# Performance work log

Hardware: AMD Instinct MI355X
Metric: run time of the kernel (lower is better)

The kernel has to match this reference:

```python
import jax, jax.numpy as jnp
import numpy as np

BETA = 0.25  # commitment weight per level (vqconfig default)
EPS = 1e-12  # F.normalize eps


def setup_inputs() -> dict:
    key = jax.random.key(0)
    k1, k2 = jax.random.split(key)
    z = jax.random.normal(k1, (4, 256, 32, 32), dtype=jnp.float32)
    cb = jax.random.normal(k2, (4, 4096, 256), dtype=jnp.float32)
    # embeddings are row-normalized at init in the torch module
    cb = cb / jnp.maximum(jnp.linalg.norm(cb, axis=-1, keepdims=True), EPS)
    return {"z": z, "codebooks": cb}


def _nearest_code(r_flat, embed):
    """use_znorm=True path: cosine-similarity nearest neighbor.
    r_flat: (N, C), embed: (K, C) -> idx: (N,) int32"""
    rn = r_flat / jnp.maximum(jnp.linalg.norm(r_flat, axis=1, keepdims=True), EPS)
    en = embed / jnp.maximum(jnp.linalg.norm(embed, axis=1, keepdims=True), EPS)
    sim = jnp.einsum('nc,kc->nk', rn, en)  # (N, K)
    return jnp.argmax(sim, axis=1)


def reference(z, codebooks):
    """Residual VQ over L codebooks (eval mode: no EMA / kmeans init).
    z: (B, C, H, W); codebooks: (L, K, C).
    Returns (z_q_st (B,C,H,W), indices (L,B,H,W), qloss scalar)."""
    B, C, H, W = z.shape
    L = codebooks.shape[0]
    z_flat = z.transpose(0, 2, 3, 1).reshape(-1, C)  # (N, C)
    residual = z_flat
    q_sum = jnp.zeros_like(z_flat)
    qloss = jnp.zeros((), dtype=z.dtype)
    indices = []
    for l in range(L):  # small fixed level loop with sequential data dependency
        E = codebooks[l]
        idx = _nearest_code(residual, E)          # (N,)
        z_q = E[idx]                              # gather (N, C)
        q_sum = q_sum + z_q
        qloss = qloss + BETA * jnp.mean((jax.lax.stop_gradient(z_q) - residual) ** 2)
        residual = residual - jax.lax.stop_gradient(z_q)
        indices.append(idx.reshape(B, H, W))
    q = q_sum.reshape(B, H, W, C).transpose(0, 3, 1, 2)
    z_q_st = z + jax.lax.stop_gradient(q - z)     # straight-through estimator
    return z_q_st, jnp.stack(indices, axis=0), qloss
```

## Files before the change

kernel.cpp:

```cpp
#include <hip/hip_runtime.h>


#define OFF_AS   0
#define OFF_BS   524288
#define OFF_R    2621440
#define OFF_INV  3670016
#define OFF_PV   3686400
#define OFF_RN   3817472
#define OFF_CNT  3821568
#define OFF_CAND 3825664
#define OFF_CVAL 4874240
#define OFF_SSQ  5922816

#define BETA 0.25f
#define EPSN 1e-12f
#define CAP 256
#define SLC 16
#define OVF (1 << 20)
#define MARGIN 0.012f
#define NEGINF -3.0e38f

typedef __attribute__((ext_vector_type(8))) short short8;
typedef __attribute__((ext_vector_type(4))) float f32x4;

__device__ __forceinline__ unsigned short f2bf(float x) {
  unsigned u = __float_as_uint(x);
  unsigned r = (u + 0x7fffu + ((u >> 16) & 1u)) >> 16;
  return (unsigned short)r;
}

__device__ __forceinline__ void gload16(const void* g, void* s) {
  __builtin_amdgcn_global_load_lds(
      (const __attribute__((address_space(1))) unsigned int*)g,
      (__attribute__((address_space(3))) unsigned int*)s, 16, 0, 0);
}

__global__ __launch_bounds__(256) void k_prep_r(const float* __restrict__ z,
                                                float* __restrict__ r) {
  __shared__ float t[32][33];
  int id = blockIdx.x;
  int b = id >> 8; int rem = id & 255; int ct = rem >> 5; int ht = rem & 31;
  int c0 = ct * 32, h0 = ht * 32;
  int col = threadIdx.x & 31, row0 = threadIdx.x >> 5;
#pragma unroll
  for (int p = 0; p < 4; ++p) {
    int row = row0 + p * 8;
    t[row][col] = z[((b * 256 + c0 + row) << 10) + h0 + col];
  }
  __syncthreads();
#pragma unroll
  for (int p = 0; p < 4; ++p) {
    int row = row0 + p * 8;
    r[(b * 1024 + h0 + row) * 256 + c0 + col] = t[col][row];
  }
}

__global__ __launch_bounds__(256) void k_prep_inv(const float* __restrict__ cb,
                                                  float* __restrict__ inv) {
  int w = threadIdx.x >> 6, lane = threadIdx.x & 63;
  int row = blockIdx.x * 4 + w;
  float4 v = *(const float4*)(cb + row * 256 + lane * 4);
  float s = v.x * v.x + v.y * v.y + v.z * v.z + v.w * v.w;
#pragma unroll
  for (int off = 32; off; off >>= 1) s += __shfl_xor(s, off);
  if (lane == 0) inv[row] = 1.0f / fmaxf(sqrtf(s), EPSN);
}

__global__ __launch_bounds__(256) void k_bsplit_all(const float* __restrict__ cb,
                                                    const float* __restrict__ inv,
                                                    unsigned short* __restrict__ BS) {
  int row = blockIdx.x, c = threadIdx.x;
  float x = cb[(row << 8) + c] * inv[row];
  BS[(row << 8) + c] = f2bf(x);
}

__global__ __launch_bounds__(256) void k_split_a(const float* __restrict__ r,
                                                 unsigned short* __restrict__ AS,
                                                 float* __restrict__ rnorm,
                                                 int* __restrict__ cnt) {
  __shared__ float wsum[4];
  int n = blockIdx.x, tid = threadIdx.x;
  float x = r[(n << 8) + tid];
  AS[(n << 8) + tid] = f2bf(x);
  float sq = x * x;
  int lane = tid & 63, w = tid >> 6;
#pragma unroll
  for (int off = 32; off; off >>= 1) sq += __shfl_xor(sq, off);
  if (lane == 0) wsum[w] = sq;
  __syncthreads();
  if (tid == 0) {
    rnorm[n] = sqrtf((wsum[0] + wsum[1]) + (wsum[2] + wsum[3]));
    cnt[n] = 0;
  }
}

__global__ __launch_bounds__(256) void k_gemm_argmax(
    const unsigned short* __restrict__ AS, const unsigned short* __restrict__ BS,
    float* __restrict__ pval, const float* __restrict__ rnorm,
    int* __restrict__ cnt, int* __restrict__ cand, float* __restrict__ cval) {
  __shared__ unsigned short lA[128 * 64];
  __shared__ unsigned short lB[128 * 64];
  __shared__ float sv[2][2][64];
  __shared__ float scomb[2][64];
  __shared__ float rn_s[2][64];
  __shared__ int   lcnt[128];
  __shared__ int   lck[128][SLC];
  __shared__ float lcv[128][SLC];

  int bid = blockIdx.x;
  int wg = (bid & 7) * 128 + (bid >> 3);
  int bm = wg >> 5, bn = wg & 31;
  int mbase = bm * 128, nbase = bn * 128;
  int tid = threadIdx.x;
  int wid = tid >> 6, ln = tid & 63;
  int wr = wid >> 1, wc = wid & 1;
  int grp = ln >> 4, li = ln & 15;

  f32x4 acc[4][4];
#pragma unroll
  for (int i = 0; i < 4; ++i)
#pragma unroll
    for (int j = 0; j < 4; ++j) acc[i][j] = (f32x4){0.f, 0.f, 0.f, 0.f};

  for (int ks = 0; ks < 4; ++ks) {
    __syncthreads();
    int k0 = ks * 64;
#pragma unroll
    for (int i = 0; i < 4; ++i) {
      int idx = i * 256 + tid;
      int row = idx >> 3, cc = idx & 7;
      int src = cc ^ (row & 7);
      gload16(AS + ((mbase + row) << 8) + k0 + src * 8, ((char*)lA) + idx * 16);
    }
#pragma unroll
    for (int i = 0; i < 4; ++i) {
      int idx = i * 256 + tid;
      int row = idx >> 3, cc = idx & 7;
      int src = cc ^ (row & 7);
      gload16(BS + ((nbase + row) << 8) + k0 + src * 8, ((char*)lB) + idx * 16);
    }
    __syncthreads();
#pragma unroll
    for (int kk = 0; kk < 2; ++kk) {
      short8 b[4];
#pragma unroll
      for (int ni = 0; ni < 4; ++ni) {
        int row = wc * 64 + ni * 16 + li;
        int cc = kk * 4 + grp;
        b[ni] = *(const short8*)(((const char*)lB) + row * 128 + (cc ^ (row & 7)) * 16);
      }
#pragma unroll
      for (int mi = 0; mi < 4; ++mi) {
        int row = wr * 64 + mi * 16 + li;
        int cc = kk * 4 + grp;
        short8 a = *(const short8*)(((const char*)lA) + row * 128 + (cc ^ (row & 7)) * 16);
#pragma unroll
        for (int ni = 0; ni < 4; ++ni)
          acc[mi][ni] = __builtin_amdgcn_mfma_f32_16x16x32_bf16(a, b[ni], acc[mi][ni], 0, 0, 0);
      }
    }
  }

#pragma unroll
  for (int mi = 0; mi < 4; ++mi) {
#pragma unroll
    for (int reg = 0; reg < 4; ++reg) {
      float v = acc[mi][0][reg];
#pragma unroll
      for (int ni = 1; ni < 4; ++ni) v = fmaxf(v, acc[mi][ni][reg]);
#pragma unroll
      for (int off = 1; off < 16; off <<= 1) v = fmaxf(v, __shfl_xor(v, off));
      if (li == 0) sv[wr][wc][mi * 16 + grp * 4 + reg] = v;
    }
  }
  __syncthreads();
  if (tid < 128) {
    int wr2 = tid >> 6, r64 = tid & 63;
    float m = fmaxf(sv[wr2][0][r64], sv[wr2][1][r64]);
    int n = mbase + wr2 * 64 + r64;
    pval[n * 32 + bn] = m;
    scomb[wr2][r64] = m;
    rn_s[wr2][r64] = rnorm[n];
    lcnt[tid] = 0;
  }
  __syncthreads();
#pragma unroll
  for (int mi = 0; mi < 4; ++mi) {
#pragma unroll
    for (int reg = 0; reg < 4; ++reg) {
      int rl = mi * 16 + grp * 4 + reg;
      float thr = scomb[wr][rl] - MARGIN * rn_s[wr][rl];
      int rloc = wr * 64 + rl;
#pragma unroll
      for (int ni = 0; ni < 4; ++ni) {
        float v = acc[mi][ni][reg];
        if (v >= thr) {
          int pos = atomicAdd(&lcnt[rloc], 1);
          if (pos < SLC) {
            lck[rloc][pos] = nbase + wc * 64 + ni * 16 + li;
            lcv[rloc][pos] = v;
          }
        }
      }
    }
  }
  __syncthreads();
  if (tid < 128) {
    int rloc = tid;
    int n = mbase + rloc;
    int raw = lcnt[rloc];
    int lc = raw < SLC ? raw : SLC;
    int add = raw > SLC ? (lc + OVF) : lc;
    if (add > 0) {
      int base = atomicAdd(&cnt[n], add);
      for (int j = 0; j < lc; ++j) {
        int pos = base + j;
        if (pos < CAP) {
          cand[n * CAP + pos] = lck[rloc][j];
          cval[n * CAP + pos] = lcv[rloc][j];
        }
      }
    }
  }
}

__global__ __launch_bounds__(256) void k_refine_update(
    const float* __restrict__ cb, const float* __restrict__ inv,
    float* __restrict__ r, const float* __restrict__ pval,
    float* __restrict__ rnorm, int* __restrict__ cnt,
    const int* __restrict__ cand, const float* __restrict__ cval,
    unsigned short* __restrict__ AS, float* __restrict__ ssq,
    float* __restrict__ out_idx, int l) {
  __shared__ float rrow[256];
  __shared__ float gm_s;
  __shared__ int list[CAP];
  __shared__ int lcnt;
  __shared__ float wbv[4];
  __shared__ int wbk[4];
  __shared__ int sbk;
  __shared__ float wsum[4];

  int n = blockIdx.x, tid = threadIdx.x;
  int w = tid >> 6, lane = tid & 63;
  rrow[tid] = r[(n << 8) + tid];
  if (tid == 0) lcnt = 0;
  if (tid < 64) {
    float v = (lane < 32) ? pval[n * 32 + lane] : NEGINF;
#pragma unroll
    for (int off = 1; off < 32; off <<= 1) v = fmaxf(v, __shfl_xor(v, off));
    if (tid == 0) gm_s = v;
  }
  __syncthreads();

  int c = cnt[n];
  const float* cbl = cb + ((size_t)l << 20);
  const float* invl = inv + (l << 12);
  float bv = NEGINF; int bk = 0x7fffffff;
  float4 rv4 = *(const float4*)(rrow + lane * 4);

  if (c <= CAP) {
    float thr = gm_s - MARGIN * rnorm[n];
    if (tid < c) {
      float v = cval[n * CAP + tid];
      if (v >= thr) { int p = atomicAdd(&lcnt, 1); list[p] = cand[n * CAP + tid]; }
    }
    __syncthreads();
    int m = lcnt;
    for (int j = w; j < m; j += 4) {
      int k = list[j];
      float4 e4 = *(const float4*)(cbl + ((size_t)k << 8) + lane * 4);
      float p = rv4.x * e4.x + rv4.y * e4.y + rv4.z * e4.z + rv4.w * e4.w;
#pragma unroll
      for (int off = 32; off; off >>= 1) p += __shfl_xor(p, off);
      float s = p * invl[k];
      if (s > bv || (s == bv && k < bk)) { bv = s; bk = k; }
    }
  } else {
    __syncthreads();
    for (int kk = 0; kk < 1024; ++kk) {
      int k = kk * 4 + w;
      float4 e4 = *(const float4*)(cbl + ((size_t)k << 8) + lane * 4);
      float p = rv4.x * e4.x + rv4.y * e4.y + rv4.z * e4.z + rv4.w * e4.w;
#pragma unroll
      for (int off = 32; off; off >>= 1) p += __shfl_xor(p, off);
      float s = p * invl[k];
      if (s > bv || (s == bv && k < bk)) { bv = s; bk = k; }
    }
  }
  if (lane == 0) { wbv[w] = bv; wbk[w] = bk; }
  __syncthreads();
  if (tid == 0) {
    float v0 = wbv[0]; int i0 = wbk[0];
#pragma unroll
    for (int ww = 1; ww < 4; ++ww) {
      float ov = wbv[ww]; int oi = wbk[ww];
      if (ov > v0 || (ov == v0 && oi < i0)) { v0 = ov; i0 = oi; }
    }
    sbk = i0;
    out_idx[(l << 12) + n] = (float)i0;
  }
  __syncthreads();

  int ii = sbk;
  float e = cbl[((size_t)ii << 8) + tid];
  float rvv = rrow[tid] - e;
  r[(n << 8) + tid] = rvv;
  AS[(n << 8) + tid] = f2bf(rvv);
  float sq = rvv * rvv;
#pragma unroll
  for (int off = 32; off; off >>= 1) sq += __shfl_xor(sq, off);
  if (lane == 0) wsum[w] = sq;
  __syncthreads();
  if (tid == 0) {
    float tot = (wsum[0] + wsum[1]) + (wsum[2] + wsum[3]);
    ssq[(l << 12) + n] = tot;
    rnorm[n] = sqrtf(tot);
    cnt[n] = 0;
  }
}

__global__ __launch_bounds__(256) void k_qloss(const float* __restrict__ ssq,
                                               float* __restrict__ out) {
  __shared__ float wsum[4];
  int tid = threadIdx.x;
  float q = 0.f;
  for (int l = 0; l < 4; ++l) {
    float p = 0.f;
#pragma unroll
    for (int i = 0; i < 16; ++i) p += ssq[l * 4096 + i * 256 + tid];
    int lane = tid & 63, w = tid >> 6;
#pragma unroll
    for (int off = 32; off; off >>= 1) p += __shfl_xor(p, off);
    if (lane == 0) wsum[w] = p;
    __syncthreads();
    float tot = (wsum[0] + wsum[1]) + (wsum[2] + wsum[3]);
    q += BETA * (tot * (1.0f / (4096.0f * 256.0f)));
    __syncthreads();
  }
  if (tid == 0) out[1048576 + 16384] = q;
}

__global__ __launch_bounds__(256) void k_writeq(const float* __restrict__ z,
                                                const float* __restrict__ r,
                                                float* __restrict__ out) {
  __shared__ float t[32][33];
  int id = blockIdx.x;
  int b = id >> 8; int rem = id & 255; int ct = rem >> 5; int ht = rem & 31;
  int c0 = ct * 32, h0 = ht * 32;
  int col = threadIdx.x & 31, row0 = threadIdx.x >> 5;
#pragma unroll
  for (int p = 0; p < 4; ++p) {
    int row = row0 + p * 8;
    t[row][col] = r[(b * 1024 + h0 + row) * 256 + c0 + col];
  }
  __syncthreads();
#pragma unroll
  for (int p = 0; p < 4; ++p) {
    int row = row0 + p * 8;
    int o = ((b * 256 + c0 + row) << 10) + h0 + col;
    out[o] = z[o] - t[col][row];
  }
}

extern "C" void kernel_launch(void* const* d_in, const int* in_sizes, int n_in,
                              void* d_out, int out_size, void* d_ws, size_t ws_size,
                              hipStream_t stream) {
  const float* z  = (const float*)d_in[0];
  const float* cb = (const float*)d_in[1];
  float* out = (float*)d_out;
  float* ws  = (float*)d_ws;

  unsigned short* AS = (unsigned short*)(ws + OFF_AS);
  unsigned short* BS = (unsigned short*)(ws + OFF_BS);
  float* r     = ws + OFF_R;
  float* inv   = ws + OFF_INV;
  float* pval  = ws + OFF_PV;
  float* rnorm = ws + OFF_RN;
  int*   cnt   = (int*)(ws + OFF_CNT);
  int*   cand  = (int*)(ws + OFF_CAND);
  float* cval  = ws + OFF_CVAL;
  float* ssq   = ws + OFF_SSQ;

  k_prep_r<<<1024, 256, 0, stream>>>(z, r);
  k_prep_inv<<<4096, 256, 0, stream>>>(cb, inv);
  k_bsplit_all<<<16384, 256, 0, stream>>>(cb, inv, BS);
  k_split_a<<<4096, 256, 0, stream>>>(r, AS, rnorm, cnt);
  for (int l = 0; l < 4; ++l) {
    k_gemm_argmax<<<1024, 256, 0, stream>>>(AS, BS + (size_t)l * 4096 * 256,
                                            pval, rnorm, cnt, cand, cval);
    k_refine_update<<<4096, 256, 0, stream>>>(cb, inv, r, pval, rnorm, cnt,
                                              cand, cval, AS, ssq,
                                              out + 1048576, l);
  }
  k_qloss<<<1, 256, 0, stream>>>(ssq, out);
  k_writeq<<<1024, 256, 0, stream>>>(z, r, out);
}
```

Measured before the change: 184.7 us.

## Fuse prep kernels and merge qloss reduction into final writeback launch

Replaces the four setup kernels with two: one that computes codebook inverse norms and bf16 normalized rows in a single pass through shared memory, and one that transposes z, writes the fp32 residual and bf16 copy, and computes row norms together. The separate qloss kernel is folded into the final transpose-writeback launch as an extra block. This cuts launch count and avoids re-reading the codebook and residual from global memory. The new row-prep kernel reads z with 8-wide strided accesses, which may coalesce less well.

```diff
diff --git a/kernel.cpp b/kernel.cpp
--- a/kernel.cpp
+++ b/kernel.cpp
@@ -21,6 +21,7 @@
 #define NEGINF -3.0e38f
 
 typedef __attribute__((ext_vector_type(8))) short short8;
+typedef __attribute__((ext_vector_type(4))) short short4v;
 typedef __attribute__((ext_vector_type(4))) float f32x4;
 
 __device__ __forceinline__ unsigned short f2bf(float x) {
@@ -35,62 +36,83 @@
       (__attribute__((address_space(3))) unsigned int*)s, 16, 0, 0);
 }
 
-__global__ __launch_bounds__(256) void k_prep_r(const float* __restrict__ z,
-                                                float* __restrict__ r) {
-  __shared__ float t[32][33];
-  int id = blockIdx.x;
-  int b = id >> 8; int rem = id & 255; int ct = rem >> 5; int ht = rem & 31;
-  int c0 = ct * 32, h0 = ht * 32;
-  int col = threadIdx.x & 31, row0 = threadIdx.x >> 5;
-#pragma unroll
-  for (int p = 0; p < 4; ++p) {
-    int row = row0 + p * 8;
-    t[row][col] = z[((b * 256 + c0 + row) << 10) + h0 + col];
-  }
-  __syncthreads();
-#pragma unroll
-  for (int p = 0; p < 4; ++p) {
-    int row = row0 + p * 8;
-    r[(b * 1024 + h0 + row) * 256 + c0 + col] = t[col][row];
-  }
-}
-
-__global__ __launch_bounds__(256) void k_prep_inv(const float* __restrict__ cb,
-                                                  float* __restrict__ inv) {
-  int w = threadIdx.x >> 6, lane = threadIdx.x & 63;
-  int row = blockIdx.x * 4 + w;
-  float4 v = *(const float4*)(cb + row * 256 + lane * 4);
-  float s = v.x * v.x + v.y * v.y + v.z * v.z + v.w * v.w;
-#pragma unroll
-  for (int off = 32; off; off >>= 1) s += __shfl_xor(s, off);
-  if (lane == 0) inv[row] = 1.0f / fmaxf(sqrtf(s), EPSN);
-}
-
-__global__ __launch_bounds__(256) void k_bsplit_all(const float* __restrict__ cb,
-                                                    const float* __restrict__ inv,
-                                                    unsigned short* __restrict__ BS) {
-  int row = blockIdx.x, c = threadIdx.x;
-  float x = cb[(row << 8) + c] * inv[row];
-  BS[(row << 8) + c] = f2bf(x);
-}
-
-__global__ __launch_bounds__(256) void k_split_a(const float* __restrict__ r,
-                                                 unsigned short* __restrict__ AS,
-                                                 float* __restrict__ rnorm,
-                                                 int* __restrict__ cnt) {
-  __shared__ float wsum[4];
-  int n = blockIdx.x, tid = threadIdx.x;
-  float x = r[(n << 8) + tid];
-  AS[(n << 8) + tid] = f2bf(x);
-  float sq = x * x;
-  int lane = tid & 63, w = tid >> 6;
-#pragma unroll
-  for (int off = 32; off; off >>= 1) sq += __shfl_xor(sq, off);
-  if (lane == 0) wsum[w] = sq;
-  __syncthreads();
-  if (tid == 0) {
-    rnorm[n] = sqrtf((wsum[0] + wsum[1]) + (wsum[2] + wsum[3]));
-    cnt[n] = 0;
+__global__ __launch_bounds__(256) void k_prep_rows(const float* __restrict__ z,
+                                                   float* __restrict__ r,
+                                                   unsigned short* __restrict__ AS,
+                                                   float* __restrict__ rnorm,
+                                                   int* __restrict__ cnt) {
+  __shared__ float t[256][9];
+  __shared__ float wpart[4][8];
+  int n0 = blockIdx.x * 8;
+  int b = n0 >> 10, hw0 = n0 & 1023;
+  int tid = threadIdx.x;
+  int w = tid >> 6, lane = tid & 63;
+#pragma unroll
+  for (int p = 0; p < 8; ++p) {
+    int c = p * 32 + (tid >> 3), h = tid & 7;
+    t[c][h] = z[((b * 256 + c) << 10) + hw0 + h];
+  }
+  __syncthreads();
+#pragma unroll
+  for (int h = 0; h < 8; ++h) {
+    float v = t[tid][h];
+    float s = v * v;
+#pragma unroll
+    for (int off = 32; off; off >>= 1) s += __shfl_xor(s, off);
+    if (lane == 0) wpart[w][h] = s;
+  }
+  __syncthreads();
+  if (tid < 8) {
+    float tot = (wpart[0][tid] + wpart[1][tid]) + (wpart[2][tid] + wpart[3][tid]);
+    rnorm[n0 + tid] = sqrtf(tot);
+    cnt[n0 + tid] = 0;
+  }
+#pragma unroll
+  for (int h = 0; h < 8; ++h) {
+    float v = t[tid][h];
+    r[(n0 + h) * 256 + tid] = v;
+    AS[(n0 + h) * 256 + tid] = f2bf(v);
+  }
+}
+
+__global__ __launch_bounds__(256) void k_prep_cb(const float* __restrict__ cb,
+                                                 float* __restrict__ inv,
+                                                 unsigned short* __restrict__ BS) {
+  __shared__ float t[8][260];
+  __shared__ float sinvs[8];
+  int r0 = blockIdx.x * 8;
+  int tid = threadIdx.x;
+  int w = tid >> 6, lane = tid & 63;
+#pragma unroll
+  for (int p = 0; p < 2; ++p) {
+    int idx = p * 1024 + tid * 4;
+    float4 v = *(const float4*)(cb + (size_t)r0 * 256 + idx);
+    int row = idx >> 8, c = idx & 255;
+    *(float4*)&t[row][c] = v;
+  }
+  __syncthreads();
+#pragma unroll
+  for (int rr = 0; rr < 2; ++rr) {
+    int row = w * 2 + rr;
+    float4 v = *(const float4*)&t[row][lane * 4];
+    float s = v.x * v.x + v.y * v.y + v.z * v.z + v.w * v.w;
+#pragma unroll
+    for (int off = 32; off; off >>= 1) s += __shfl_xor(s, off);
+    if (lane == 0) sinvs[row] = 1.0f / fmaxf(sqrtf(s), EPSN);
+  }
+  __syncthreads();
+  if (tid < 8) inv[r0 + tid] = sinvs[tid];
+#pragma unroll
+  for (int p = 0; p < 2; ++p) {
+    int idx = p * 1024 + tid * 4;
+    int row = idx >> 8, c = idx & 255;
+    float sc = sinvs[row];
+    short4v s4;
+    s4[0] = (short)f2bf(t[row][c + 0] * sc);
+    s4[1] = (short)f2bf(t[row][c + 1] * sc);
+    s4[2] = (short)f2bf(t[row][c + 2] * sc);
+    s4[3] = (short)f2bf(t[row][c + 3] * sc);
+    *(short4v*)(BS + (size_t)r0 * 256 + idx) = s4;
   }
 }
 
@@ -319,35 +341,35 @@
   }
 }
 
-__global__ __launch_bounds__(256) void k_qloss(const float* __restrict__ ssq,
-                                               float* __restrict__ out) {
-  __shared__ float wsum[4];
+__global__ __launch_bounds__(256) void k_writeq_qloss(const float* __restrict__ z,
+                                                      const float* __restrict__ r,
+                                                      const float* __restrict__ ssq,
+                                                      float* __restrict__ out) {
   int tid = threadIdx.x;
-  float q = 0.f;
-  for (int l = 0; l < 4; ++l) {
-    float p = 0.f;
-#pragma unroll
-    for (int i = 0; i < 16; ++i) p += ssq[l * 4096 + i * 256 + tid];
-    int lane = tid & 63, w = tid >> 6;
-#pragma unroll
-    for (int off = 32; off; off >>= 1) p += __shfl_xor(p, off);
-    if (lane == 0) wsum[w] = p;
-    __syncthreads();
-    float tot = (wsum[0] + wsum[1]) + (wsum[2] + wsum[3]);
-    q += BETA * (tot * (1.0f / (4096.0f * 256.0f)));
-    __syncthreads();
-  }
-  if (tid == 0) out[1048576 + 16384] = q;
-}
-
-__global__ __launch_bounds__(256) void k_writeq(const float* __restrict__ z,
-                                                const float* __restrict__ r,
-                                                float* __restrict__ out) {
+  if (blockIdx.x == 1024) {
+    __shared__ float wsumq[4];
+    float q = 0.f;
+    for (int l = 0; l < 4; ++l) {
+      float p = 0.f;
+#pragma unroll
+      for (int i = 0; i < 16; ++i) p += ssq[l * 4096 + i * 256 + tid];
+      int lane = tid & 63, w = tid >> 6;
+#pragma unroll
+      for (int off = 32; off; off >>= 1) p += __shfl_xor(p, off);
+      if (lane == 0) wsumq[w] = p;
+      __syncthreads();
+      float tot = (wsumq[0] + wsumq[1]) + (wsumq[2] + wsumq[3]);
+      q += BETA * (tot * (1.0f / (4096.0f * 256.0f)));
+      __syncthreads();
+    }
+    if (tid == 0) out[1048576 + 16384] = q;
+    return;
+  }
   __shared__ float t[32][33];
   int id = blockIdx.x;
   int b = id >> 8; int rem = id & 255; int ct = rem >> 5; int ht = rem & 31;
   int c0 = ct * 32, h0 = ht * 32;
-  int col = threadIdx.x & 31, row0 = threadIdx.x >> 5;
+  int col = tid & 31, row0 = tid >> 5;
 #pragma unroll
   for (int p = 0; p < 4; ++p) {
     int row = row0 + p * 8;
@@ -381,10 +403,8 @@
   float* cval  = ws + OFF_CVAL;
   float* ssq   = ws + OFF_SSQ;
 
-  k_prep_r<<<1024, 256, 0, stream>>>(z, r);
-  k_prep_inv<<<4096, 256, 0, stream>>>(cb, inv);
-  k_bsplit_all<<<16384, 256, 0, stream>>>(cb, inv, BS);
-  k_split_a<<<4096, 256, 0, stream>>>(r, AS, rnorm, cnt);
+  k_prep_cb<<<2048, 256, 0, stream>>>(cb, inv, BS);
+  k_prep_rows<<<512, 256, 0, stream>>>(z, r, AS, rnorm, cnt);
   for (int l = 0; l < 4; ++l) {
     k_gemm_argmax<<<1024, 256, 0, stream>>>(AS, BS + (size_t)l * 4096 * 256,
                                             pval, rnorm, cnt, cand, cval);
@@ -392,6 +412,5 @@
                                               cand, cval, AS, ssq,
                                               out + 1048576, l);
   }
-  k_qloss<<<1, 256, 0, stream>>>(ssq, out);
-  k_writeq<<<1024, 256, 0, stream>>>(z, r, out);
-}
+  k_writeq_qloss<<<1025, 256, 0, stream>>>(z, r, ssq, out);
+}
```

Measured after the change: 178.5 us. -3.4%, faster.
